# Kernel tuning notes

Measured on AMD Instinct MI355X. Metric: run time of the kernel, lower is better.

Reference implementation:

```python
import jax, jax.numpy as jnp
import numpy as np

KS = 7
PAD = (KS - 1) // 2


def setup_inputs() -> dict:
    key = jax.random.key(0)
    k1, k2 = jax.random.split(key)
    x = jax.random.normal(k1, (16, 64, 256, 256), dtype=jnp.float32)
    conv_w = jax.random.normal(k2, (1, 2, KS, KS), dtype=jnp.float32) * 0.1
    conv_b = jnp.zeros((1,), dtype=jnp.float32)
    return {"x": x, "conv_w": conv_w, "conv_b": conv_b}


def reference(x, conv_w, conv_b):
    # channel-wise mean and max -> [B, 2, H, W]
    avg_mask = jnp.mean(x, axis=1, keepdims=True)
    max_mask = jnp.max(x, axis=1, keepdims=True)
    mask = jnp.concatenate([avg_mask, max_mask], axis=1)
    # tiny 2->1 conv, 'same' padding
    mask = jax.lax.conv_general_dilated(
        mask, conv_w,
        window_strides=(1, 1),
        padding=[(PAD, PAD), (PAD, PAD)],
        dimension_numbers=("NCHW", "OIHW", "NCHW"),
    ) + conv_b[None, :, None, None]
    mask = jax.nn.sigmoid(mask)
    return x * mask
```

## Files before the change

### kernel.cpp

```cpp
#include <hip/hip_runtime.h>

static constexpr int B = 16, C = 64, H = 256, W = 256;
static constexpr int HW = H * W;
static constexpr int KS = 7, PAD = 3;

typedef float f4 __attribute__((ext_vector_type(4)));

__global__ void __launch_bounds__(256) reduce_mean_max(
    const float* __restrict__ x, float* __restrict__ avg, float* __restrict__ mx)
{
    int idx = blockIdx.x * 256 + threadIdx.x;
    int b   = idx >> 14;
    const f4* xp = reinterpret_cast<const f4*>(x)
                 + (size_t)b * (C * (HW / 4)) + (idx & (HW / 4 - 1));
    f4 v = xp[0];
    f4 s = v;
    f4 a = v;
    #pragma unroll 8
    for (int c = 1; c < C; ++c) {
        f4 t = xp[(size_t)c * (HW / 4)];
        s += t;
        a.x = fmaxf(a.x, t.x); a.y = fmaxf(a.y, t.y);
        a.z = fmaxf(a.z, t.z); a.w = fmaxf(a.w, t.w);
    }
    const float inv = 1.0f / C;
    reinterpret_cast<f4*>(avg)[idx] = s * inv;
    reinterpret_cast<f4*>(mx)[idx]  = a;
}

__global__ void __launch_bounds__(256) conv_sigmoid(
    const float* __restrict__ avg, const float* __restrict__ mx,
    const float* __restrict__ wgt, const float* __restrict__ bias,
    float* __restrict__ mask)
{
    constexpr int TS = 16;
    constexpr int TI = TS + KS - 1;
    __shared__ float sa[TI][24];
    __shared__ float sm[TI][24];

    const int tx = threadIdx.x & 15;
    const int ty = threadIdx.x >> 4;
    const int w0 = blockIdx.x * TS;
    const int h0 = blockIdx.y * TS;
    const int b  = blockIdx.z;

    const float* ap = avg + (size_t)b * HW;
    const float* mp = mx  + (size_t)b * HW;

    for (int e = threadIdx.x; e < TI * TI; e += 256) {
        int r = e / TI, c = e % TI;
        int gh = h0 + r - PAD, gw = w0 + c - PAD;
        bool ok = ((unsigned)gh < (unsigned)H) && ((unsigned)gw < (unsigned)W);
        int gi = gh * W + gw;
        sa[r][c] = ok ? ap[gi] : 0.0f;
        sm[r][c] = ok ? mp[gi] : 0.0f;
    }
    __syncthreads();

    float acc = bias[0];
    #pragma unroll
    for (int ky = 0; ky < KS; ++ky) {
        #pragma unroll
        for (int kx = 0; kx < KS; ++kx) {
            acc += sa[ty + ky][tx + kx] * wgt[ky * KS + kx];
            acc += sm[ty + ky][tx + kx] * wgt[49 + ky * KS + kx];
        }
    }
    float s = 1.0f / (1.0f + expf(-acc));
    mask[(size_t)b * HW + (h0 + ty) * W + (w0 + tx)] = s;
}

__global__ void __launch_bounds__(256) apply_mask(
    const float* __restrict__ x, const float* __restrict__ mask,
    float* __restrict__ out)
{
    int idx = blockIdx.x * 256 + threadIdx.x;
    int b   = idx >> 20;
    int hw4 = idx & (HW / 4 - 1);
    f4 xv = reinterpret_cast<const f4*>(x)[idx];
    f4 mv = reinterpret_cast<const f4*>(mask)[(b << 14) + hw4];
    f4 r  = xv * mv;
    __builtin_nontemporal_store(r, reinterpret_cast<f4*>(out) + idx);
}

extern "C" void kernel_launch(void* const* d_in, const int* in_sizes, int n_in,
                              void* d_out, int out_size, void* d_ws, size_t ws_size,
                              hipStream_t stream) {
    const float* x      = (const float*)d_in[0];
    const float* conv_w = (const float*)d_in[1];
    const float* conv_b = (const float*)d_in[2];
    float* out  = (float*)d_out;

    float* avg  = (float*)d_ws;
    float* mx   = avg + (size_t)B * HW;
    float* mask = mx  + (size_t)B * HW;

    reduce_mean_max<<<(B * HW / 4) / 256, 256, 0, stream>>>(x, avg, mx);

    dim3 cgrid(W / 16, H / 16, B);
    conv_sigmoid<<<cgrid, 256, 0, stream>>>(avg, mx, conv_w, conv_b, mask);

    apply_mask<<<(B * C * HW / 4) / 256, 256, 0, stream>>>(x, mask, out);
}
```

Before: 143.4 us.

## Fuse conv-sigmoid with mask multiply and chunk batches for L2 reuse

Merges the conv+sigmoid and apply-mask kernels into one kernel. Each block computes the mask for 4 full rows and then multiplies all 64 channels of x for those rows, so the mask never goes through global memory. The batch is also processed in chunks of 8, so the x slice read by the reduction may still sit in cache when the fused kernel reads it again. In exchange there are more launches, and each fused block redundantly loads a 10-row halo and does serial conv work before streaming x.

```diff
diff --git a/kernel.cpp b/kernel.cpp
--- a/kernel.cpp
+++ b/kernel.cpp
@@ -3,16 +3,18 @@
 static constexpr int B = 16, C = 64, H = 256, W = 256;
 static constexpr int HW = H * W;
 static constexpr int KS = 7, PAD = 3;
+static constexpr int CH = 8;
 
 typedef float f4 __attribute__((ext_vector_type(4)));
 
 __global__ void __launch_bounds__(256) reduce_mean_max(
-    const float* __restrict__ x, float* __restrict__ avg, float* __restrict__ mx)
+    const float* __restrict__ x, float* __restrict__ avg, float* __restrict__ mx,
+    int b0)
 {
     int idx = blockIdx.x * 256 + threadIdx.x;
-    int b   = idx >> 14;
-    const f4* xp = reinterpret_cast<const f4*>(x)
-                 + (size_t)b * (C * (HW / 4)) + (idx & (HW / 4 - 1));
+    int b   = b0 + (idx >> 14);
+    int p   = idx & (HW / 4 - 1);
+    const f4* xp = reinterpret_cast<const f4*>(x) + (size_t)b * (C * (HW / 4)) + p;
     f4 v = xp[0];
     f4 s = v;
     f4 a = v;
@@ -24,63 +26,67 @@
         a.z = fmaxf(a.z, t.z); a.w = fmaxf(a.w, t.w);
     }
     const float inv = 1.0f / C;
-    reinterpret_cast<f4*>(avg)[idx] = s * inv;
-    reinterpret_cast<f4*>(mx)[idx]  = a;
+    size_t o = (size_t)b * (HW / 4) + p;
+    reinterpret_cast<f4*>(avg)[o] = s * inv;
+    reinterpret_cast<f4*>(mx)[o]  = a;
 }
 
-__global__ void __launch_bounds__(256) conv_sigmoid(
-    const float* __restrict__ avg, const float* __restrict__ mx,
-    const float* __restrict__ wgt, const float* __restrict__ bias,
-    float* __restrict__ mask)
+__global__ void __launch_bounds__(256) conv_mul(
+    const float* __restrict__ x, const float* __restrict__ avg,
+    const float* __restrict__ mx, const float* __restrict__ wgt,
+    const float* __restrict__ bias, float* __restrict__ out, int b0)
 {
-    constexpr int TS = 16;
-    constexpr int TI = TS + KS - 1;
-    __shared__ float sa[TI][24];
-    __shared__ float sm[TI][24];
+    __shared__ float sa[10][264];
+    __shared__ float sm[10][264];
+    __shared__ float smask[4][256];
+    __shared__ float sw[2][49];
+    __shared__ float sbias;
 
-    const int tx = threadIdx.x & 15;
-    const int ty = threadIdx.x >> 4;
-    const int w0 = blockIdx.x * TS;
-    const int h0 = blockIdx.y * TS;
-    const int b  = blockIdx.z;
+    const int t  = threadIdx.x;
+    const int h0 = blockIdx.x * 4;
+    const int b  = b0 + blockIdx.y;
+
+    if (t < 98) ((float*)sw)[t] = wgt[t];
+    if (t == 98) sbias = bias[0];
 
     const float* ap = avg + (size_t)b * HW;
     const float* mp = mx  + (size_t)b * HW;
-
-    for (int e = threadIdx.x; e < TI * TI; e += 256) {
-        int r = e / TI, c = e % TI;
-        int gh = h0 + r - PAD, gw = w0 + c - PAD;
+    for (int e = t; e < 10 * 262; e += 256) {
+        int r = e / 262, ci = e % 262;
+        int gh = h0 + r - PAD, gw = ci - PAD;
         bool ok = ((unsigned)gh < (unsigned)H) && ((unsigned)gw < (unsigned)W);
         int gi = gh * W + gw;
-        sa[r][c] = ok ? ap[gi] : 0.0f;
-        sm[r][c] = ok ? mp[gi] : 0.0f;
+        sa[r][ci] = ok ? ap[gi] : 0.0f;
+        sm[r][ci] = ok ? mp[gi] : 0.0f;
     }
     __syncthreads();
 
-    float acc = bias[0];
     #pragma unroll
-    for (int ky = 0; ky < KS; ++ky) {
+    for (int r = 0; r < 4; ++r) {
+        float acc = sbias;
         #pragma unroll
-        for (int kx = 0; kx < KS; ++kx) {
-            acc += sa[ty + ky][tx + kx] * wgt[ky * KS + kx];
-            acc += sm[ty + ky][tx + kx] * wgt[49 + ky * KS + kx];
+        for (int ky = 0; ky < KS; ++ky) {
+            #pragma unroll
+            for (int kx = 0; kx < KS; ++kx) {
+                acc += sa[r + ky][t + kx] * sw[0][ky * KS + kx];
+                acc += sm[r + ky][t + kx] * sw[1][ky * KS + kx];
+            }
         }
+        smask[r][t] = 1.0f / (1.0f + expf(-acc));
     }
-    float s = 1.0f / (1.0f + expf(-acc));
-    mask[(size_t)b * HW + (h0 + ty) * W + (w0 + tx)] = s;
-}
+    __syncthreads();
 
-__global__ void __launch_bounds__(256) apply_mask(
-    const float* __restrict__ x, const float* __restrict__ mask,
-    float* __restrict__ out)
-{
-    int idx = blockIdx.x * 256 + threadIdx.x;
-    int b   = idx >> 20;
-    int hw4 = idx & (HW / 4 - 1);
-    f4 xv = reinterpret_cast<const f4*>(x)[idx];
-    f4 mv = reinterpret_cast<const f4*>(mask)[(b << 14) + hw4];
-    f4 r  = xv * mv;
-    __builtin_nontemporal_store(r, reinterpret_cast<f4*>(out) + idx);
+    const int row = t >> 6;
+    const int q   = t & 63;
+    f4 mv = reinterpret_cast<const f4*>(&smask[row][0])[q];
+    size_t base = (((size_t)b * C) * H + (h0 + row)) * (W / 4) + q;
+    const f4* xp = reinterpret_cast<const f4*>(x)   + base;
+    f4*       op = reinterpret_cast<f4*>(out)       + base;
+    #pragma unroll 8
+    for (int c = 0; c < C; ++c) {
+        f4 xv = xp[(size_t)c * (H * (W / 4))];
+        __builtin_nontemporal_store(xv * mv, op + (size_t)c * (H * (W / 4)));
+    }
 }
 
 extern "C" void kernel_launch(void* const* d_in, const int* in_sizes, int n_in,
@@ -93,12 +99,11 @@
 
     float* avg  = (float*)d_ws;
     float* mx   = avg + (size_t)B * HW;
-    float* mask = mx  + (size_t)B * HW;
 
-    reduce_mean_max<<<(B * HW / 4) / 256, 256, 0, stream>>>(x, avg, mx);
-
-    dim3 cgrid(W / 16, H / 16, B);
-    conv_sigmoid<<<cgrid, 256, 0, stream>>>(avg, mx, conv_w, conv_b, mask);
-
-    apply_mask<<<(B * C * HW / 4) / 256, 256, 0, stream>>>(x, mask, out);
+    for (int chunk = 0; chunk < B / CH; ++chunk) {
+        int b0 = chunk * CH;
+        reduce_mean_max<<<(CH * HW / 4) / 256, 256, 0, stream>>>(x, avg, mx, b0);
+        dim3 g(H / 4, CH);
+        conv_mul<<<g, 256, 0, stream>>>(x, avg, mx, conv_w, conv_b, out, b0);
+    }
 }
```

Result: slower. 156.3 us (+9.0%).

## Stash a bf16 copy of x during reduction and apply the mask from it

Applied to the files above, without the earlier changes.

The reduction pass now reads x with nontemporal loads and also writes a bfloat16 copy of every element. The final multiply reads that half-size copy instead of re-reading the fp32 input. The aim is a smaller second read that may stay resident in the large last-level cache. Total DRAM traffic is nominally unchanged, the output loses precision to bf16 rounding of x, and the path only runs when the workspace is large enough.

```diff
diff --git a/kernel.cpp b/kernel.cpp
--- a/kernel.cpp
+++ b/kernel.cpp
@@ -5,6 +5,40 @@
 static constexpr int KS = 7, PAD = 3;
 
 typedef float f4 __attribute__((ext_vector_type(4)));
+typedef unsigned short u16x4 __attribute__((ext_vector_type(4)));
+typedef unsigned short u16x8 __attribute__((ext_vector_type(8)));
+
+__device__ __forceinline__ unsigned short f2bf(float f) {
+    unsigned u = __float_as_uint(f);
+    return (unsigned short)((u + 0x7FFFu + ((u >> 16) & 1u)) >> 16);
+}
+
+__global__ void __launch_bounds__(256) reduce_stash(
+    const float* __restrict__ x, float* __restrict__ avg, float* __restrict__ mx,
+    unsigned short* __restrict__ xh)
+{
+    int idx = blockIdx.x * 256 + threadIdx.x;
+    int b   = idx >> 14;
+    int p   = idx & (HW / 4 - 1);
+    const f4* xp = reinterpret_cast<const f4*>(x) + (size_t)b * (C * (HW / 4)) + p;
+    u16x4*    hp = reinterpret_cast<u16x4*>(xh)   + (size_t)b * (C * (HW / 4)) + p;
+    f4 s = {0.f, 0.f, 0.f, 0.f};
+    f4 a = {-INFINITY, -INFINITY, -INFINITY, -INFINITY};
+    #pragma unroll 8
+    for (int c = 0; c < C; ++c) {
+        f4 t = __builtin_nontemporal_load(xp + (size_t)c * (HW / 4));
+        s += t;
+        a.x = fmaxf(a.x, t.x); a.y = fmaxf(a.y, t.y);
+        a.z = fmaxf(a.z, t.z); a.w = fmaxf(a.w, t.w);
+        u16x4 h;
+        h.x = f2bf(t.x); h.y = f2bf(t.y); h.z = f2bf(t.z); h.w = f2bf(t.w);
+        hp[(size_t)c * (HW / 4)] = h;
+    }
+    const float inv = 1.0f / C;
+    size_t o = (size_t)b * (HW / 4) + p;
+    reinterpret_cast<f4*>(avg)[o] = s * inv;
+    reinterpret_cast<f4*>(mx)[o]  = a;
+}
 
 __global__ void __launch_bounds__(256) reduce_mean_max(
     const float* __restrict__ x, float* __restrict__ avg, float* __restrict__ mx)
@@ -14,8 +48,7 @@
     const f4* xp = reinterpret_cast<const f4*>(x)
                  + (size_t)b * (C * (HW / 4)) + (idx & (HW / 4 - 1));
     f4 v = xp[0];
-    f4 s = v;
-    f4 a = v;
+    f4 s = v, a = v;
     #pragma unroll 8
     for (int c = 1; c < C; ++c) {
         f4 t = xp[(size_t)c * (HW / 4)];
@@ -70,6 +103,30 @@
     mask[(size_t)b * HW + (h0 + ty) * W + (w0 + tx)] = s;
 }
 
+__global__ void __launch_bounds__(256) apply_stash(
+    const unsigned short* __restrict__ xh, const float* __restrict__ mask,
+    float* __restrict__ out)
+{
+    int idx = blockIdx.x * 256 + threadIdx.x;
+    int b   = idx >> 19;
+    int hw8 = idx & (HW / 8 - 1);
+    u16x8 hv = reinterpret_cast<const u16x8*>(xh)[idx];
+    const f4* mp = reinterpret_cast<const f4*>(mask) + ((size_t)b << 14) + 2 * hw8;
+    f4 m0 = mp[0], m1 = mp[1];
+    f4 x0, x1;
+    x0.x = __uint_as_float((unsigned)hv[0] << 16);
+    x0.y = __uint_as_float((unsigned)hv[1] << 16);
+    x0.z = __uint_as_float((unsigned)hv[2] << 16);
+    x0.w = __uint_as_float((unsigned)hv[3] << 16);
+    x1.x = __uint_as_float((unsigned)hv[4] << 16);
+    x1.y = __uint_as_float((unsigned)hv[5] << 16);
+    x1.z = __uint_as_float((unsigned)hv[6] << 16);
+    x1.w = __uint_as_float((unsigned)hv[7] << 16);
+    f4* op = reinterpret_cast<f4*>(out) + 2 * (size_t)idx;
+    __builtin_nontemporal_store(x0 * m0, op);
+    __builtin_nontemporal_store(x1 * m1, op + 1);
+}
+
 __global__ void __launch_bounds__(256) apply_mask(
     const float* __restrict__ x, const float* __restrict__ mask,
     float* __restrict__ out)
@@ -79,8 +136,7 @@
     int hw4 = idx & (HW / 4 - 1);
     f4 xv = reinterpret_cast<const f4*>(x)[idx];
     f4 mv = reinterpret_cast<const f4*>(mask)[(b << 14) + hw4];
-    f4 r  = xv * mv;
-    __builtin_nontemporal_store(r, reinterpret_cast<f4*>(out) + idx);
+    __builtin_nontemporal_store(xv * mv, reinterpret_cast<f4*>(out) + idx);
 }
 
 extern "C" void kernel_launch(void* const* d_in, const int* in_sizes, int n_in,
@@ -94,11 +150,22 @@
     float* avg  = (float*)d_ws;
     float* mx   = avg + (size_t)B * HW;
     float* mask = mx  + (size_t)B * HW;
+    unsigned short* xh = (unsigned short*)(mask + (size_t)B * HW);
 
-    reduce_mean_max<<<(B * HW / 4) / 256, 256, 0, stream>>>(x, avg, mx);
+    const size_t need = (size_t)3 * B * HW * sizeof(float)
+                      + (size_t)B * C * HW * sizeof(unsigned short);
+    const bool stash = ws_size >= need;
+
+    if (stash)
+        reduce_stash<<<(B * HW / 4) / 256, 256, 0, stream>>>(x, avg, mx, xh);
+    else
+        reduce_mean_max<<<(B * HW / 4) / 256, 256, 0, stream>>>(x, avg, mx);
 
     dim3 cgrid(W / 16, H / 16, B);
     conv_sigmoid<<<cgrid, 256, 0, stream>>>(avg, mx, conv_w, conv_b, mask);
 
-    apply_mask<<<(B * C * HW / 4) / 256, 256, 0, stream>>>(x, mask, out);
+    if (stash)
+        apply_stash<<<(B * C * HW / 8) / 256, 256, 0, stream>>>(xh, mask, out);
+    else
+        apply_mask<<<(B * C * HW / 4) / 256, 256, 0, stream>>>(x, mask, out);
 }
```

New measurement: 181.2 us. 1.26x slower.
